# Kernel tuning notes

Hardware: AMD Instinct MI355X
Metric: run time of the kernel (lower is better)

Reference implementation:

```python
import jax, jax.numpy as jnp
import numpy as np

B, TQ, TK = 2, 2048, 2048
D_IN, D_OUT, H = 1024, 1024, 16
HD = D_OUT // H  # head dim = 64


def setup_inputs() -> dict:
    key = jax.random.key(0)
    ks = jax.random.split(key, 11)
    s = 1.0 / np.sqrt(D_IN)
    so = 1.0 / np.sqrt(D_OUT)
    return {
        "q": jax.random.normal(ks[0], (B, TQ, D_IN), jnp.float32),
        "k": jax.random.normal(ks[1], (B, TK, D_IN), jnp.float32),
        "v": jax.random.normal(ks[2], (B, TK, D_IN), jnp.float32),
        "Wq": jax.random.uniform(ks[3], (D_OUT, D_IN), jnp.float32, -s, s),
        "bq": jax.random.uniform(ks[4], (D_OUT,), jnp.float32, -s, s),
        "Wk": jax.random.uniform(ks[5], (D_OUT, D_IN), jnp.float32, -s, s),
        "bk": jax.random.uniform(ks[6], (D_OUT,), jnp.float32, -s, s),
        "Wv": jax.random.uniform(ks[7], (D_OUT, D_IN), jnp.float32, -s, s),
        "bv": jax.random.uniform(ks[8], (D_OUT,), jnp.float32, -s, s),
        "Wo": jax.random.uniform(ks[9], (D_OUT, D_OUT), jnp.float32, -so, so),
        "bo": jax.random.uniform(ks[10], (D_OUT,), jnp.float32, -so, so),
    }


def reference(q, k, v, Wq, bq, Wk, bk, Wv, bv, Wo, bo):
    b, tq, _ = q.shape
    tk = k.shape[1]
    # linear projections, split heads: [B,T,D] -> [B,H,T,HD]
    qh = (q @ Wq.T + bq).reshape(b, tq, H, HD).transpose(0, 2, 1, 3)
    kh = (k @ Wk.T + bk).reshape(b, tk, H, HD).transpose(0, 2, 1, 3)
    vh = (v @ Wv.T + bv).reshape(b, tk, H, HD).transpose(0, 2, 1, 3)
    # scaled dot-product attention (forward never applies the causal mask)
    scores = jnp.einsum("bhqd,bhkd->bhqk", qh, kh) / np.sqrt(HD).astype(np.float32)
    attn = jax.nn.softmax(scores, axis=-1)
    x = jnp.einsum("bhqk,bhkd->bhqd", attn, vh)
    x = x.transpose(0, 2, 1, 3).reshape(b, tq, D_OUT)
    return x @ Wo.T + bo
```

## Files before the change

kernel.cpp:

```cpp
#include <hip/hip_runtime.h>
#include <hip/hip_bf16.h>

typedef __bf16 b16x8 __attribute__((ext_vector_type(8)));
typedef unsigned short u16x8 __attribute__((ext_vector_type(8)));
typedef unsigned short u16x4 __attribute__((ext_vector_type(4)));
typedef unsigned int u32x4 __attribute__((ext_vector_type(4)));
typedef float f32x4 __attribute__((ext_vector_type(4)));
typedef float f32x16 __attribute__((ext_vector_type(16)));

__device__ __forceinline__ unsigned short f2b(float f) {
  unsigned u = __builtin_bit_cast(unsigned, f);
  u += 0x7fff + ((u >> 16) & 1);
  return (unsigned short)(u >> 16);
}

__device__ __forceinline__ b16x8 as_b(u16x8 v) { return __builtin_bit_cast(b16x8, v); }

__device__ __forceinline__ float fexp2(float x) {
#if __has_builtin(__builtin_amdgcn_exp2f)
  return __builtin_amdgcn_exp2f(x);
#else
  return exp2f(x);
#endif
}

__device__ __forceinline__ unsigned pk2(float lo, float hi) {
  return (unsigned)f2b(lo) | ((unsigned)f2b(hi) << 16);
}

__device__ __forceinline__ void plswap(unsigned& a, unsigned& b) {
  asm volatile("v_permlane32_swap_b32 %0, %1" : "+v"(a), "+v"(b));
}

__device__ __forceinline__ b16x8 mkchunk(float p0, float p1, float p2, float p3,
                                         float p4, float p5, float p6, float p7) {
  unsigned a1 = pk2(p0, p1), b1 = pk2(p4, p5);
  unsigned a2 = pk2(p2, p3), b2 = pk2(p6, p7);
  plswap(a1, b1);
  plswap(a2, b2);
  u32x4 w = {a1, a2, b1, b2};
  return __builtin_bit_cast(b16x8, w);
}

#define AS1 __attribute__((address_space(1)))
#define AS3 __attribute__((address_space(3)))
__device__ __forceinline__ void gload_lds16(const void* g, void* l) {
  __builtin_amdgcn_global_load_lds((const AS1 void*)g, (AS3 void*)l, 16, 0, 0);
}


__global__ __launch_bounds__(256) void convert_kernel(
    const float* __restrict__ q, const float* __restrict__ k, const float* __restrict__ v,
    const float* __restrict__ Wq, const float* __restrict__ Wk,
    const float* __restrict__ Wv, const float* __restrict__ Wo,
    unsigned short* __restrict__ qb, unsigned short* __restrict__ kb,
    unsigned short* __restrict__ vb, unsigned short* __restrict__ wqb,
    unsigned short* __restrict__ wkb, unsigned short* __restrict__ wvb,
    unsigned short* __restrict__ wob) {
  const float* src; unsigned short* dst; int rows;
  switch (blockIdx.y) {
    case 0: src = q;  dst = qb;  rows = 4096; break;
    case 1: src = k;  dst = kb;  rows = 4096; break;
    case 2: src = v;  dst = vb;  rows = 4096; break;
    case 3: src = Wq; dst = wqb; rows = 1024; break;
    case 4: src = Wk; dst = wkb; rows = 1024; break;
    case 5: src = Wv; dst = wvb; rows = 1024; break;
    default: src = Wo; dst = wob; rows = 1024; break;
  }
  const int row = blockIdx.x * 2 + (threadIdx.x >> 7);
  if (row >= rows) return;
  const int t = threadIdx.x & 127;
  const float* sp = src + (size_t)row * 1024 + t * 8;
  float4 f0 = *(const float4*)sp;
  float4 f1 = *(const float4*)(sp + 4);
  u16x8 h = { f2b(f0.x), f2b(f0.y), f2b(f0.z), f2b(f0.w),
              f2b(f1.x), f2b(f1.y), f2b(f1.z), f2b(f1.w) };
  const int swcol = ((t >> 3) << 6) | (((t & 7) ^ (row & 7)) << 3);
  *(u16x8*)(dst + (size_t)row * 1024 + swcol) = h;
}

template <int MODE, typename TOUT>
__device__ __forceinline__ void gemm_body(unsigned short* sA, unsigned short* sB,
                                          const unsigned short* __restrict__ A,
                                          const unsigned short* __restrict__ Bm,
                                          const float* __restrict__ bias,
                                          TOUT* __restrict__ C) {
  const int tid = threadIdx.x;
  const int l = tid & 63, w = tid >> 6;
  const int wm = w >> 1, wn = w & 1;
  const int lr = l & 15, lg = l >> 4;
  const int bm = blockIdx.y * 64, bn = blockIdx.x * 128;
  const int r8 = l >> 3, sl = l & 7;

  f32x4 acc[2][4] = {};

  for (int k0 = 0; k0 < 1024; k0 += 64) {
#pragma unroll
    for (int i = 0; i < 2; ++i) {
      const int row = i * 32 + w * 8 + r8;
      gload_lds16(A + (size_t)(bm + row) * 1024 + k0 + sl * 8, &sA[i * 2048 + w * 512]);
    }
#pragma unroll
    for (int i = 0; i < 4; ++i) {
      const int row = i * 32 + w * 8 + r8;
      gload_lds16(Bm + (size_t)(bn + row) * 1024 + k0 + sl * 8, &sB[i * 2048 + w * 512]);
    }
    __syncthreads();

    b16x8 af[2][2], bf[4][2];
#pragma unroll
    for (int mb = 0; mb < 2; ++mb)
#pragma unroll
      for (int kh = 0; kh < 2; ++kh) {
        const int r = wm * 32 + mb * 16 + lr;
        af[mb][kh] = as_b(*(const u16x8*)(&sA[(r * 64 + kh * 32 + lg * 8) ^ ((r & 7) << 3)]));
      }
#pragma unroll
    for (int nb = 0; nb < 4; ++nb)
#pragma unroll
      for (int kh = 0; kh < 2; ++kh) {
        const int r = wn * 64 + nb * 16 + lr;
        bf[nb][kh] = as_b(*(const u16x8*)(&sB[(r * 64 + kh * 32 + lg * 8) ^ ((r & 7) << 3)]));
      }
#pragma unroll
    for (int mb = 0; mb < 2; ++mb)
#pragma unroll
      for (int nb = 0; nb < 4; ++nb) {
        acc[mb][nb] = __builtin_amdgcn_mfma_f32_16x16x32_bf16(af[mb][0], bf[nb][0], acc[mb][nb], 0, 0, 0);
        acc[mb][nb] = __builtin_amdgcn_mfma_f32_16x16x32_bf16(af[mb][1], bf[nb][1], acc[mb][nb], 0, 0, 0);
      }
    __syncthreads();
  }

  const float qscale = 0.125f * 1.44269504f;
#pragma unroll
  for (int mb = 0; mb < 2; ++mb)
#pragma unroll
    for (int nb = 0; nb < 4; ++nb) {
      const int c = bn + wn * 64 + nb * 16 + lr;
      const float bv = bias[c];
      const int r0 = bm + wm * 32 + mb * 16 + lg * 4;
      if constexpr (MODE == 2) {
        const int hh = c >> 6, hd = c & 63;
        const int bb = r0 >> 11, t0 = r0 & 2047;
        u16x4 pk = { f2b(acc[mb][nb][0] + bv), f2b(acc[mb][nb][1] + bv),
                     f2b(acc[mb][nb][2] + bv), f2b(acc[mb][nb][3] + bv) };
        const int tsw = (t0 & ~63) | (((((t0 >> 3) & 7) ^ (hd & 7)) << 3)) | (t0 & 7);
        *(u16x4*)(&C[(((size_t)bb * 16 + hh) * 64 + hd) * 2048 + tsw]) = pk;
      } else {
#pragma unroll
        for (int i = 0; i < 4; ++i) {
          float val = acc[mb][nb][i] + bv;
          if constexpr (MODE == 1) val *= qscale;
          if constexpr (MODE == 3) {
            C[(size_t)(r0 + i) * 1024 + c] = val;
          } else {
            const int cc = (c & ~63) | (((((c >> 3) & 7) ^ ((r0 + i) & 7)) << 3)) | (c & 7);
            C[(size_t)(r0 + i) * 1024 + cc] = (TOUT)f2b(val);
          }
        }
      }
    }
}

__global__ __launch_bounds__(256) void proj_kernel(
    const unsigned short* __restrict__ qb, const unsigned short* __restrict__ kb,
    const unsigned short* __restrict__ vb,
    const unsigned short* __restrict__ wqb, const float* __restrict__ bq,
    const unsigned short* __restrict__ wkb, const float* __restrict__ bk,
    const unsigned short* __restrict__ wvb, const float* __restrict__ bv,
    unsigned short* __restrict__ Qh, unsigned short* __restrict__ Kh,
    unsigned short* __restrict__ Vt) {
  __shared__ __align__(16) unsigned short sA[64 * 64];
  __shared__ __align__(16) unsigned short sB[128 * 64];
  if (blockIdx.z == 0)      gemm_body<1, unsigned short>(sA, sB, qb, wqb, bq, Qh);
  else if (blockIdx.z == 1) gemm_body<0, unsigned short>(sA, sB, kb, wkb, bk, Kh);
  else                      gemm_body<2, unsigned short>(sA, sB, vb, wvb, bv, Vt);
}

__global__ __launch_bounds__(256) void out_kernel(
    const unsigned short* __restrict__ X, const unsigned short* __restrict__ wob,
    const float* __restrict__ bo, float* __restrict__ out) {
  __shared__ __align__(16) unsigned short sA[64 * 64];
  __shared__ __align__(16) unsigned short sB[128 * 64];
  gemm_body<3, float>(sA, sB, X, wob, bo, out);
}

__global__ __launch_bounds__(256, 2) void attn_kernel(
    const unsigned short* __restrict__ Qh, const unsigned short* __restrict__ Kh,
    const unsigned short* __restrict__ Vt, unsigned short* __restrict__ X) {
  __shared__ __align__(16) unsigned short sK[2][64 * 64];
  __shared__ __align__(16) unsigned short sV[2][64 * 64];

  const int tid = threadIdx.x;
  const int l = tid & 63, wq = tid >> 6;
  const int lq = l & 31, lg = l >> 5;
  const int b = blockIdx.y >> 4, h = blockIdx.y & 15;
  const int q0 = blockIdx.x * 128 + wq * 32;

  const size_t baseQK = (size_t)b * 2048 * 1024 + (size_t)h * 64;
  const size_t baseV  = ((size_t)(b * 16 + h)) * 64 * 2048;

  const int rk = lq & 7;
  b16x8 qf0, qf1, qf2, qf3;
  {
    const unsigned short* qp = Qh + baseQK + (size_t)(q0 + lq) * 1024;
    qf0 = as_b(*(const u16x8*)(qp + (((0 + lg) ^ rk) << 3)));
    qf1 = as_b(*(const u16x8*)(qp + (((2 + lg) ^ rk) << 3)));
    qf2 = as_b(*(const u16x8*)(qp + (((4 + lg) ^ rk) << 3)));
    qf3 = as_b(*(const u16x8*)(qp + (((6 + lg) ^ rk) << 3)));
  }

  const int r8 = l >> 3, sl = l & 7;

  auto stage = [&](int buf, int kv0) {
#pragma unroll
    for (int i = 0; i < 2; ++i) {
      const int rowb = 16 * wq + 8 * i;
      gload_lds16(Kh + baseQK + (size_t)(kv0 + rowb + r8) * 1024 + sl * 8, &sK[buf][rowb * 64]);
      gload_lds16(Vt + baseV + (size_t)(rowb + r8) * 2048 + kv0 + sl * 8, &sV[buf][rowb * 64]);
    }
  };

  float m_run = -1e30f, l_run = 0.f;
  f32x16 Oa = {}, Ob = {};

  stage(0, 0);
  __syncthreads();

  for (int t = 0; t < 32; ++t) {
    const int cur = t & 1;
    if (t + 1 < 32) stage(cur ^ 1, (t + 1) * 64);

    const unsigned short* K_ = sK[cur];
    const unsigned short* V_ = sV[cur];
    const int sw = (lq & 7) << 3;

    f32x16 s0 = {}, s1 = {};
#pragma unroll
    for (int c = 0; c < 4; ++c) {
      const int hd8 = c * 16 + 8 * lg;
      b16x8 kf0 = as_b(*(const u16x8*)(&K_[lq * 64 + (hd8 ^ sw)]));
      b16x8 kf1 = as_b(*(const u16x8*)(&K_[(32 + lq) * 64 + (hd8 ^ sw)]));
      b16x8 qf = (c == 0) ? qf0 : (c == 1) ? qf1 : (c == 2) ? qf2 : qf3;
      s0 = __builtin_amdgcn_mfma_f32_32x32x16_bf16(kf0, qf, s0, 0, 0, 0);
      s1 = __builtin_amdgcn_mfma_f32_32x32x16_bf16(kf1, qf, s1, 0, 0, 0);
    }

    float mx = s0[0];
#pragma unroll
    for (int j = 1; j < 16; ++j) mx = fmaxf(mx, s0[j]);
#pragma unroll
    for (int j = 0; j < 16; ++j) mx = fmaxf(mx, s1[j]);
    mx = fmaxf(mx, __shfl_xor(mx, 32));
    const float mnew = fmaxf(m_run, mx);
    const float al = fexp2(m_run - mnew);
    m_run = mnew;
    float rs = 0.f;
#pragma unroll
    for (int j = 0; j < 16; ++j) { s0[j] = fexp2(s0[j] - mnew); rs += s0[j]; }
#pragma unroll
    for (int j = 0; j < 16; ++j) { s1[j] = fexp2(s1[j] - mnew); rs += s1[j]; }
    rs += __shfl_xor(rs, 32);
    l_run = l_run * al + rs;
#pragma unroll
    for (int j = 0; j < 16; ++j) { Oa[j] *= al; Ob[j] *= al; }

    b16x8 pb0 = mkchunk(s0[0], s0[1], s0[2], s0[3], s0[4], s0[5], s0[6], s0[7]);
    b16x8 pb1 = mkchunk(s0[8], s0[9], s0[10], s0[11], s0[12], s0[13], s0[14], s0[15]);
    b16x8 pb2 = mkchunk(s1[0], s1[1], s1[2], s1[3], s1[4], s1[5], s1[6], s1[7]);
    b16x8 pb3 = mkchunk(s1[8], s1[9], s1[10], s1[11], s1[12], s1[13], s1[14], s1[15]);

#pragma unroll
    for (int c = 0; c < 4; ++c) {
      const int kv8 = c * 16 + 8 * lg;
      b16x8 vfa = as_b(*(const u16x8*)(&V_[lq * 64 + (kv8 ^ sw)]));
      b16x8 vfb = as_b(*(const u16x8*)(&V_[(32 + lq) * 64 + (kv8 ^ sw)]));
      b16x8 pb = (c == 0) ? pb0 : (c == 1) ? pb1 : (c == 2) ? pb2 : pb3;
      Oa = __builtin_amdgcn_mfma_f32_32x32x16_bf16(vfa, pb, Oa, 0, 0, 0);
      Ob = __builtin_amdgcn_mfma_f32_32x32x16_bf16(vfb, pb, Ob, 0, 0, 0);
    }
    __syncthreads();
  }

  const float inv = 1.0f / l_run;
  unsigned short* xp = X + baseQK + (size_t)(q0 + lq) * 1024;
#pragma unroll
  for (int g = 0; g < 4; ++g) {
    u16x4 wa = { f2b(Oa[4 * g + 0] * inv), f2b(Oa[4 * g + 1] * inv),
                 f2b(Oa[4 * g + 2] * inv), f2b(Oa[4 * g + 3] * inv) };
    *(u16x4*)(xp + ((g ^ rk) << 3) + 4 * lg) = wa;
    u16x4 wb = { f2b(Ob[4 * g + 0] * inv), f2b(Ob[4 * g + 1] * inv),
                 f2b(Ob[4 * g + 2] * inv), f2b(Ob[4 * g + 3] * inv) };
    *(u16x4*)(xp + (((4 + g) ^ rk) << 3) + 4 * lg) = wb;
  }
}

extern "C" void kernel_launch(void* const* d_in, const int* in_sizes, int n_in,
                              void* d_out, int out_size, void* d_ws, size_t ws_size,
                              hipStream_t stream) {
  const float* q  = (const float*)d_in[0];
  const float* k  = (const float*)d_in[1];
  const float* v  = (const float*)d_in[2];
  const float* Wq = (const float*)d_in[3];
  const float* bq = (const float*)d_in[4];
  const float* Wk = (const float*)d_in[5];
  const float* bk = (const float*)d_in[6];
  const float* Wv = (const float*)d_in[7];
  const float* bv = (const float*)d_in[8];
  const float* Wo = (const float*)d_in[9];
  const float* bo = (const float*)d_in[10];

  unsigned short* ws = (unsigned short*)d_ws;
  const size_t M1 = (size_t)1024 * 1024;
  unsigned short* qb  = ws;
  unsigned short* kb  = ws + 4 * M1;
  unsigned short* vb  = ws + 8 * M1;
  unsigned short* wqb = ws + 12 * M1;
  unsigned short* wkb = ws + 13 * M1;
  unsigned short* wvb = ws + 14 * M1;
  unsigned short* wob = ws + 15 * M1;
  unsigned short* Qh  = ws + 16 * M1;
  unsigned short* Kh  = ws + 20 * M1;
  unsigned short* Vt  = ws + 24 * M1;
  unsigned short* X   = qb;

  dim3 blk(256);
  convert_kernel<<<dim3(2048, 7), blk, 0, stream>>>(q, k, v, Wq, Wk, Wv, Wo,
                                                    qb, kb, vb, wqb, wkb, wvb, wob);
  proj_kernel<<<dim3(8, 64, 3), blk, 0, stream>>>(qb, kb, vb, wqb, bq, wkb, bk, wvb, bv,
                                                  Qh, Kh, Vt);
  attn_kernel<<<dim3(16, 32), blk, 0, stream>>>(Qh, Kh, Vt, X);
  out_kernel<<<dim3(8, 64), blk, 0, stream>>>(X, wob, bo, (float*)d_out);
}
```

Before: 143.6 us.

## Use hardware bf16 pack, lazy softmax rescale, tree reductions and MFMA priority

Replaces the software round-to-nearest bf16 packing with the v_cvt_pk_bf16_f32 instruction in the P-chunk build and the output store. The online softmax now skips the running-max update and the O/l rescale unless some lane's new max exceeds the running max by more than 8 (log2 units), which removes most per-tile rescale multiplies. Max and sum reductions become balanced trees for more instruction-level parallelism, and s_setprio raises wave priority around the MFMA blocks. The lazy rescale lets exponentials grow up to 2^8 before renormalising, which could affect precision or overflow for unusual inputs.

```diff
diff --git a/kernel.cpp b/kernel.cpp
--- a/kernel.cpp
+++ b/kernel.cpp
@@ -5,6 +5,7 @@
 typedef unsigned short u16x8 __attribute__((ext_vector_type(8)));
 typedef unsigned short u16x4 __attribute__((ext_vector_type(4)));
 typedef unsigned int u32x4 __attribute__((ext_vector_type(4)));
+typedef unsigned int u32x2 __attribute__((ext_vector_type(2)));
 typedef float f32x4 __attribute__((ext_vector_type(4)));
 typedef float f32x16 __attribute__((ext_vector_type(16)));
 
@@ -24,8 +25,10 @@
 #endif
 }
 
-__device__ __forceinline__ unsigned pk2(float lo, float hi) {
-  return (unsigned)f2b(lo) | ((unsigned)f2b(hi) << 16);
+__device__ __forceinline__ unsigned cvtpk(float lo, float hi) {
+  unsigned r;
+  asm("v_cvt_pk_bf16_f32 %0, %1, %2" : "=v"(r) : "v"(lo), "v"(hi));
+  return r;
 }
 
 __device__ __forceinline__ void plswap(unsigned& a, unsigned& b) {
@@ -34,8 +37,8 @@
 
 __device__ __forceinline__ b16x8 mkchunk(float p0, float p1, float p2, float p3,
                                          float p4, float p5, float p6, float p7) {
-  unsigned a1 = pk2(p0, p1), b1 = pk2(p4, p5);
-  unsigned a2 = pk2(p2, p3), b2 = pk2(p6, p7);
+  unsigned a1 = cvtpk(p0, p1), b1 = cvtpk(p4, p5);
+  unsigned a2 = cvtpk(p2, p3), b2 = cvtpk(p6, p7);
   plswap(a1, b1);
   plswap(a2, b2);
   u32x4 w = {a1, a2, b1, b2};
@@ -237,6 +240,7 @@
     const int sw = (lq & 7) << 3;
 
     f32x16 s0 = {}, s1 = {};
+    __builtin_amdgcn_s_setprio(1);
 #pragma unroll
     for (int c = 0; c < 4; ++c) {
       const int hd8 = c * 16 + 8 * lg;
@@ -246,31 +250,48 @@
       s0 = __builtin_amdgcn_mfma_f32_32x32x16_bf16(kf0, qf, s0, 0, 0, 0);
       s1 = __builtin_amdgcn_mfma_f32_32x32x16_bf16(kf1, qf, s1, 0, 0, 0);
     }
-
-    float mx = s0[0];
-#pragma unroll
-    for (int j = 1; j < 16; ++j) mx = fmaxf(mx, s0[j]);
-#pragma unroll
-    for (int j = 0; j < 16; ++j) mx = fmaxf(mx, s1[j]);
+    __builtin_amdgcn_s_setprio(0);
+
+    float a0 = fmaxf(fmaxf(s0[0], s0[1]), fmaxf(s0[2], s0[3]));
+    float a1 = fmaxf(fmaxf(s0[4], s0[5]), fmaxf(s0[6], s0[7]));
+    float a2 = fmaxf(fmaxf(s0[8], s0[9]), fmaxf(s0[10], s0[11]));
+    float a3 = fmaxf(fmaxf(s0[12], s0[13]), fmaxf(s0[14], s0[15]));
+    float a4 = fmaxf(fmaxf(s1[0], s1[1]), fmaxf(s1[2], s1[3]));
+    float a5 = fmaxf(fmaxf(s1[4], s1[5]), fmaxf(s1[6], s1[7]));
+    float a6 = fmaxf(fmaxf(s1[8], s1[9]), fmaxf(s1[10], s1[11]));
+    float a7 = fmaxf(fmaxf(s1[12], s1[13]), fmaxf(s1[14], s1[15]));
+    float mx = fmaxf(fmaxf(fmaxf(a0, a1), fmaxf(a2, a3)),
+                     fmaxf(fmaxf(a4, a5), fmaxf(a6, a7)));
     mx = fmaxf(mx, __shfl_xor(mx, 32));
-    const float mnew = fmaxf(m_run, mx);
-    const float al = fexp2(m_run - mnew);
-    m_run = mnew;
-    float rs = 0.f;
-#pragma unroll
-    for (int j = 0; j < 16; ++j) { s0[j] = fexp2(s0[j] - mnew); rs += s0[j]; }
-#pragma unroll
-    for (int j = 0; j < 16; ++j) { s1[j] = fexp2(s1[j] - mnew); rs += s1[j]; }
+
+    if (__any(mx > m_run + 8.0f)) {
+      const float mnew = fmaxf(m_run, mx);
+      const float al = fexp2(m_run - mnew);
+      m_run = mnew;
+      l_run *= al;
+#pragma unroll
+      for (int j = 0; j < 16; ++j) { Oa[j] *= al; Ob[j] *= al; }
+    }
+
+#pragma unroll
+    for (int j = 0; j < 16; ++j) s0[j] = fexp2(s0[j] - m_run);
+#pragma unroll
+    for (int j = 0; j < 16; ++j) s1[j] = fexp2(s1[j] - m_run);
+
+    float r0 = ((s0[0] + s0[1]) + (s0[2] + s0[3])) + ((s0[4] + s0[5]) + (s0[6] + s0[7]));
+    float r1 = ((s0[8] + s0[9]) + (s0[10] + s0[11])) + ((s0[12] + s0[13]) + (s0[14] + s0[15]));
+    float r2 = ((s1[0] + s1[1]) + (s1[2] + s1[3])) + ((s1[4] + s1[5]) + (s1[6] + s1[7]));
+    float r3 = ((s1[8] + s1[9]) + (s1[10] + s1[11])) + ((s1[12] + s1[13]) + (s1[14] + s1[15]));
+    float rs = (r0 + r1) + (r2 + r3);
     rs += __shfl_xor(rs, 32);
-    l_run = l_run * al + rs;
-#pragma unroll
-    for (int j = 0; j < 16; ++j) { Oa[j] *= al; Ob[j] *= al; }
+    l_run += rs;
 
     b16x8 pb0 = mkchunk(s0[0], s0[1], s0[2], s0[3], s0[4], s0[5], s0[6], s0[7]);
     b16x8 pb1 = mkchunk(s0[8], s0[9], s0[10], s0[11], s0[12], s0[13], s0[14], s0[15]);
     b16x8 pb2 = mkchunk(s1[0], s1[1], s1[2], s1[3], s1[4], s1[5], s1[6], s1[7]);
     b16x8 pb3 = mkchunk(s1[8], s1[9], s1[10], s1[11], s1[12], s1[13], s1[14], s1[15]);
 
+    __builtin_amdgcn_s_setprio(1);
 #pragma unroll
     for (int c = 0; c < 4; ++c) {
       const int kv8 = c * 16 + 8 * lg;
@@ -280,6 +301,7 @@
       Oa = __builtin_amdgcn_mfma_f32_32x32x16_bf16(vfa, pb, Oa, 0, 0, 0);
       Ob = __builtin_amdgcn_mfma_f32_32x32x16_bf16(vfb, pb, Ob, 0, 0, 0);
     }
+    __builtin_amdgcn_s_setprio(0);
     __syncthreads();
   }
 
@@ -287,12 +309,12 @@
   unsigned short* xp = X + baseQK + (size_t)(q0 + lq) * 1024;
 #pragma unroll
   for (int g = 0; g < 4; ++g) {
-    u16x4 wa = { f2b(Oa[4 * g + 0] * inv), f2b(Oa[4 * g + 1] * inv),
-                 f2b(Oa[4 * g + 2] * inv), f2b(Oa[4 * g + 3] * inv) };
-    *(u16x4*)(xp + ((g ^ rk) << 3) + 4 * lg) = wa;
-    u16x4 wb = { f2b(Ob[4 * g + 0] * inv), f2b(Ob[4 * g + 1] * inv),
-                 f2b(Ob[4 * g + 2] * inv), f2b(Ob[4 * g + 3] * inv) };
-    *(u16x4*)(xp + (((4 + g) ^ rk) << 3) + 4 * lg) = wb;
+    u32x2 wa = { cvtpk(Oa[4 * g + 0] * inv, Oa[4 * g + 1] * inv),
+                 cvtpk(Oa[4 * g + 2] * inv, Oa[4 * g + 3] * inv) };
+    *(u32x2*)(xp + ((g ^ rk) << 3) + 4 * lg) = wa;
+    u32x2 wb = { cvtpk(Ob[4 * g + 0] * inv, Ob[4 * g + 1] * inv),
+                 cvtpk(Ob[4 * g + 2] * inv, Ob[4 * g + 3] * inv) };
+    *(u32x2*)(xp + (((4 + g) ^ rk) << 3) + 4 * lg) = wb;
   }
 }
 
```

Result: faster. 138.0 us (-3.9%).
